# Kernel optimization log

Measured on AMD Instinct MI355X. Metric: run time of the kernel, lower is better.

## Reference

```python
import jax, jax.numpy as jnp
import numpy as np

N_STREAKS = 40  # fixed draw from num_streaks=(20, 60)


def setup_inputs() -> dict:
    key = jax.random.key(0)
    k1, k2, k3, k4, k5 = jax.random.split(key, 5)
    B, C, H, W = 32, 3, 512, 512
    x = jax.random.uniform(k1, (B, C, H, W), dtype=jnp.float32)  # images in [0,1]
    # alpha ~ U(0.15, 0.5) as in the module
    alpha = 0.15 + 0.35 * jax.random.uniform(k2, (1,), dtype=jnp.float32)
    xc = jax.random.randint(k3, (N_STREAKS,), 0, W)            # column center in [0, W-1]
    y0 = jax.random.randint(k4, (N_STREAKS,), 0, H // 2 + 1)   # top in [0, H/2]
    y1_off = jax.random.randint(k5, (N_STREAKS,), 0, H // 2 + 1)  # y1 = H/2 + y1_off in [H/2, H]
    return {"x": x, "alpha": alpha, "xc": xc, "y0": y0, "y1_off": y1_off}


def reference(x, alpha, xc, y0, y1_off):
    # Each streak applies v -> v*(1-a) + a on its rectangle; repeated k times this is
    # v*(1-a)^k + (1 - (1-a)^k), which is order-independent, so we rasterize an
    # overlap-count map K[H,W] and apply the closed-form blend in one fused pass.
    B, C, H, W = x.shape
    a = alpha[0]
    y1 = y1_off + H // 2
    rows = jnp.arange(H)
    cols = jnp.arange(W)
    row_mask = (rows[None, :] >= y0[:, None]) & (rows[None, :] < y1[:, None])  # [n, H]
    c0 = jnp.maximum(xc - 1, 0)
    col_mask = (cols[None, :] >= c0[:, None]) & (cols[None, :] < (xc + 1)[:, None])  # [n, W]
    K = jnp.einsum('nh,nw->hw', row_mask.astype(x.dtype), col_mask.astype(x.dtype))  # [H, W]
    f = jnp.power(1.0 - a, K)  # (1-a)^K, broadcast over B, C
    out = jnp.clip(x * f + (1.0 - f), 0.0, 1.0)
    return out
```

## Files before the change

kernel.cpp:

```cpp
#include <hip/hip_runtime.h>

#define IMG_H 512
#define IMG_W 512
#define MAX_STREAKS 64

__global__ void __launch_bounds__(256)
rain_factor_kernel(const float* __restrict__ alpha,
                   const int* __restrict__ xc,
                   const int* __restrict__ y0,
                   const int* __restrict__ y1_off,
                   float* __restrict__ f,
                   int n_streaks) {
    __shared__ int s_xc[MAX_STREAKS], s_y0[MAX_STREAKS], s_y1[MAX_STREAKS];
    int tid = threadIdx.x;
    if (tid < n_streaks) {
        s_xc[tid] = xc[tid];
        s_y0[tid] = y0[tid];
        s_y1[tid] = y1_off[tid] + IMG_H / 2;
    }
    __syncthreads();

    float l2f = __log2f(1.0f - alpha[0]);

    int idx = blockIdx.x * blockDim.x + threadIdx.x;
    if (idx >= IMG_H * IMG_W) return;
    int h = idx >> 9;
    int w = idx & (IMG_W - 1);

    int k = 0;
    #pragma unroll 8
    for (int s = 0; s < n_streaks; ++s) {
        int c  = s_xc[s];
        int c0 = c - 1 > 0 ? c - 1 : 0;
        int hit = (h >= s_y0[s]) & (h < s_y1[s]) & (w >= c0) & (w < c + 1);
        k += hit;
    }
    f[idx] = exp2f(l2f * (float)k);
}

__global__ void __launch_bounds__(256)
rain_apply_kernel(const float4* __restrict__ x,
                  const float4* __restrict__ f,
                  float4* __restrict__ out,
                  int n4) {
    const int fmask = (IMG_H * IMG_W / 4) - 1;
    int stride = gridDim.x * blockDim.x;
    for (int i = blockIdx.x * blockDim.x + threadIdx.x; i < n4; i += stride) {
        float4 xv = x[i];
        float4 fv = f[i & fmask];
        float4 o;
        o.x = fminf(fmaxf(fmaf(xv.x, fv.x, 1.0f - fv.x), 0.0f), 1.0f);
        o.y = fminf(fmaxf(fmaf(xv.y, fv.y, 1.0f - fv.y), 0.0f), 1.0f);
        o.z = fminf(fmaxf(fmaf(xv.z, fv.z, 1.0f - fv.z), 0.0f), 1.0f);
        o.w = fminf(fmaxf(fmaf(xv.w, fv.w, 1.0f - fv.w), 0.0f), 1.0f);
        out[i] = o;
    }
}

extern "C" void kernel_launch(void* const* d_in, const int* in_sizes, int n_in,
                              void* d_out, int out_size, void* d_ws, size_t ws_size,
                              hipStream_t stream) {
    const float* x      = (const float*)d_in[0];
    const float* alpha  = (const float*)d_in[1];
    const int*   xc     = (const int*)d_in[2];
    const int*   y0     = (const int*)d_in[3];
    const int*   y1_off = (const int*)d_in[4];
    float* out = (float*)d_out;
    float* f   = (float*)d_ws;

    int n_streaks = in_sizes[2];

    {
        int threads = 256;
        int blocks = (IMG_H * IMG_W + threads - 1) / threads;
        rain_factor_kernel<<<blocks, threads, 0, stream>>>(alpha, xc, y0, y1_off, f, n_streaks);
    }

    {
        int n4 = out_size / 4;
        int threads = 256;
        int blocks = 2048;
        rain_apply_kernel<<<blocks, threads, 0, stream>>>(
            (const float4*)x, (const float4*)f, (float4*)out, n4);
    }
}
```

Baseline: 39.13 us.

## Fuse factor rasterization into apply kernel with per-block shared-memory histogram

Replaces the two-kernel pipeline (factor map in workspace, then a grid-stride blend) with one fused kernel. Each block handles 8 rows of one image-channel plane and builds the overlap counts for those rows in LDS by scattering streak hits with shared atomics. It then converts the counts to (1-a)^K in place and blends 1024 float4s using nontemporal stores. This removes the workspace round trip and the second launch, but the per-row factor work is now repeated for every batch and channel plane, and each block carries 16KB of LDS and several barriers.

```diff
diff --git a/kernel.cpp b/kernel.cpp
--- a/kernel.cpp
+++ b/kernel.cpp
@@ -3,57 +3,71 @@
 #define IMG_H 512
 #define IMG_W 512
 #define MAX_STREAKS 64
+#define ROWS_PER_BLOCK 8
+
+typedef float v4f __attribute__((ext_vector_type(4)));
+
+__device__ __forceinline__ v4f blend4(v4f xv, v4f fv) {
+    v4f o;
+    o.x = fminf(fmaxf(fmaf(xv.x, fv.x, 1.0f - fv.x), 0.0f), 1.0f);
+    o.y = fminf(fmaxf(fmaf(xv.y, fv.y, 1.0f - fv.y), 0.0f), 1.0f);
+    o.z = fminf(fmaxf(fmaf(xv.z, fv.z, 1.0f - fv.z), 0.0f), 1.0f);
+    o.w = fminf(fmaxf(fmaf(xv.w, fv.w, 1.0f - fv.w), 0.0f), 1.0f);
+    return o;
+}
 
 __global__ void __launch_bounds__(256)
-rain_factor_kernel(const float* __restrict__ alpha,
-                   const int* __restrict__ xc,
-                   const int* __restrict__ y0,
-                   const int* __restrict__ y1_off,
-                   float* __restrict__ f,
-                   int n_streaks) {
+rain_fused_kernel(const v4f* __restrict__ x,
+                  const float* __restrict__ alpha,
+                  const int* __restrict__ xc,
+                  const int* __restrict__ y0,
+                  const int* __restrict__ y1_off,
+                  v4f* __restrict__ out,
+                  int n_streaks) {
     __shared__ int s_xc[MAX_STREAKS], s_y0[MAX_STREAKS], s_y1[MAX_STREAKS];
-    int tid = threadIdx.x;
+    __shared__ float s_f[ROWS_PER_BLOCK][IMG_W];
+    int* s_hist = (int*)&s_f[0][0];
+
+    const int tid = threadIdx.x;
     if (tid < n_streaks) {
         s_xc[tid] = xc[tid];
         s_y0[tid] = y0[tid];
         s_y1[tid] = y1_off[tid] + IMG_H / 2;
     }
+    #pragma unroll
+    for (int i = tid; i < ROWS_PER_BLOCK * IMG_W; i += 256) s_hist[i] = 0;
     __syncthreads();
 
-    float l2f = __log2f(1.0f - alpha[0]);
+    const int hbase = (blockIdx.x * ROWS_PER_BLOCK) & (IMG_H - 1);
 
-    int idx = blockIdx.x * blockDim.x + threadIdx.x;
-    if (idx >= IMG_H * IMG_W) return;
-    int h = idx >> 9;
-    int w = idx & (IMG_W - 1);
+    for (int p = tid; p < (n_streaks << 3); p += 256) {
+        int r = p & 7, s = p >> 3;
+        int h = hbase + r;
+        if (h >= s_y0[s] && h < s_y1[s]) {
+            int c = s_xc[s];
+            atomicAdd(&s_hist[(r << 9) + (c - 1 > 0 ? c - 1 : 0)], 1);
+            if (c >= 1) atomicAdd(&s_hist[(r << 9) + c], 1);
+        }
+    }
+    __syncthreads();
 
-    int k = 0;
-    #pragma unroll 8
-    for (int s = 0; s < n_streaks; ++s) {
-        int c  = s_xc[s];
-        int c0 = c - 1 > 0 ? c - 1 : 0;
-        int hit = (h >= s_y0[s]) & (h < s_y1[s]) & (w >= c0) & (w < c + 1);
-        k += hit;
+    const float l2f = __log2f(1.0f - alpha[0]);
+    #pragma unroll
+    for (int i = tid; i < ROWS_PER_BLOCK * IMG_W; i += 256) {
+        int k = s_hist[i];
+        ((float*)s_hist)[i] = exp2f(l2f * (float)k);
     }
-    f[idx] = exp2f(l2f * (float)k);
-}
+    __syncthreads();
 
-__global__ void __launch_bounds__(256)
-rain_apply_kernel(const float4* __restrict__ x,
-                  const float4* __restrict__ f,
-                  float4* __restrict__ out,
-                  int n4) {
-    const int fmask = (IMG_H * IMG_W / 4) - 1;
-    int stride = gridDim.x * blockDim.x;
-    for (int i = blockIdx.x * blockDim.x + threadIdx.x; i < n4; i += stride) {
-        float4 xv = x[i];
-        float4 fv = f[i & fmask];
-        float4 o;
-        o.x = fminf(fmaxf(fmaf(xv.x, fv.x, 1.0f - fv.x), 0.0f), 1.0f);
-        o.y = fminf(fmaxf(fmaf(xv.y, fv.y, 1.0f - fv.y), 0.0f), 1.0f);
-        o.z = fminf(fmaxf(fmaf(xv.z, fv.z, 1.0f - fv.z), 0.0f), 1.0f);
-        o.w = fminf(fmaxf(fmaf(xv.w, fv.w, 1.0f - fv.w), 0.0f), 1.0f);
-        out[i] = o;
+    const v4f* xb = x + (size_t)blockIdx.x * 1024;
+    v4f*       ob = out + (size_t)blockIdx.x * 1024;
+    const v4f* fb = (const v4f*)&s_f[0][0];
+    #pragma unroll
+    for (int k = 0; k < 4; ++k) {
+        int idx = (k << 8) + tid;
+        v4f xv = xb[idx];
+        v4f fv = fb[idx];
+        __builtin_nontemporal_store(blend4(xv, fv), &ob[idx]);
     }
 }
 
@@ -66,21 +80,10 @@
     const int*   y0     = (const int*)d_in[3];
     const int*   y1_off = (const int*)d_in[4];
     float* out = (float*)d_out;
-    float* f   = (float*)d_ws;
 
     int n_streaks = in_sizes[2];
 
-    {
-        int threads = 256;
-        int blocks = (IMG_H * IMG_W + threads - 1) / threads;
-        rain_factor_kernel<<<blocks, threads, 0, stream>>>(alpha, xc, y0, y1_off, f, n_streaks);
-    }
-
-    {
-        int n4 = out_size / 4;
-        int threads = 256;
-        int blocks = 2048;
-        rain_apply_kernel<<<blocks, threads, 0, stream>>>(
-            (const float4*)x, (const float4*)f, (float4*)out, n4);
-    }
+    int blocks = out_size / (ROWS_PER_BLOCK * IMG_W);
+    rain_fused_kernel<<<blocks, 256, 0, stream>>>(
+        (const v4f*)x, alpha, xc, y0, y1_off, (v4f*)out, n_streaks);
 }
```

Result: faster. 36.36 us (-7.1%).
